# Kernel tuning notes

Measured on AMD Instinct MI355X. Metric: run time of the kernel, lower is better.

Reference implementation:

```python
import jax, jax.numpy as jnp
import numpy as np

VOCAB, EMB, HID = 32000, 512, 512
BATCH, SEQ = 32, 512


def setup_inputs() -> dict:
    key = jax.random.key(0)
    ks = jax.random.split(key, 6)
    return {
        "enc_input": jax.random.randint(ks[0], (BATCH, SEQ), 0, VOCAB),
        "emb": jax.random.normal(ks[1], (VOCAB, EMB), dtype=jnp.float32) * 0.02,
        "W_ih": jax.random.normal(ks[2], (2, 3 * HID, EMB), dtype=jnp.float32) * 0.05,
        "W_hh": jax.random.normal(ks[3], (2, 3 * HID, HID), dtype=jnp.float32) * 0.05,
        "b_ih": jax.random.normal(ks[4], (2, 3 * HID), dtype=jnp.float32) * 0.05,
        "b_hh": jax.random.normal(ks[5], (2, 3 * HID), dtype=jnp.float32) * 0.05,
    }


def _gru_dir(gx, W_hh_d, b_hh_d, H):
    # gx: [B, S, 3H] precomputed input gates; scan left-to-right over S.
    B = gx.shape[0]

    def step(h, gxt):
        gh = h @ W_hh_d.T + b_hh_d  # [B, 3H]
        r = jax.nn.sigmoid(gxt[:, :H] + gh[:, :H])
        z = jax.nn.sigmoid(gxt[:, H:2 * H] + gh[:, H:2 * H])
        n = jnp.tanh(gxt[:, 2 * H:] + r * gh[:, 2 * H:])
        h_new = (1.0 - z) * n + z * h
        return h_new, h_new

    h0 = jnp.zeros((B, H), dtype=gx.dtype)
    hT, ys = jax.lax.scan(step, h0, jnp.swapaxes(gx, 0, 1))  # ys: [S, B, H]
    return jnp.swapaxes(ys, 0, 1), hT


def reference(enc_input, emb, W_ih, W_hh, b_ih, b_hh):
    # NOTE: original torch code feeds the bidirectional GRU one timestep at a
    # time, so BOTH directions effectively run left-to-right over the sequence
    # (each with its own weights). We reproduce that exact behavior.
    H = W_hh.shape[-1]
    x = emb[enc_input]  # [B, S, E]
    # Precompute input-gate projections for both directions in one einsum.
    gx = jnp.einsum('bse,dge->bsdg', x, W_ih) + b_ih  # [B, S, 2, 3H]
    out0, h0 = _gru_dir(gx[:, :, 0, :], W_hh[0], b_hh[0], H)
    out1, h1 = _gru_dir(gx[:, :, 1, :], W_hh[1], b_hh[1], H)
    encoded = jnp.concatenate([out0, out1], axis=-1)  # [B, S, 2H]
    hidden = jnp.stack([h0, h1], axis=0)  # [2, B, H]
    return encoded, hidden
```

## Files before the change

### kernel.cpp

```cpp
#include <hip/hip_runtime.h>
#include <stdint.h>

#define VOCAB 32000
#define EMBD 512
#define HID 512
#define BATCH 32
#define SEQL 512

typedef short bf16x8 __attribute__((ext_vector_type(8)));
typedef short bf16x4 __attribute__((ext_vector_type(4)));
typedef float f32x4 __attribute__((ext_vector_type(4)));

#define AGENT __HIP_MEMORY_SCOPE_AGENT
#define RLX __ATOMIC_RELAXED

static __device__ __forceinline__ float bf2f(short u) {
  union { unsigned u; float f; } c;
  c.u = ((unsigned)(unsigned short)u) << 16;
  return c.f;
}
static __device__ __forceinline__ unsigned short f2bf(float f) {
  union { float f; unsigned u; } c;
  c.f = f;
  unsigned x = c.u;
  unsigned r = (x + 0x7fffu + ((x >> 16) & 1u)) >> 16;
  return (unsigned short)r;
}

__global__ __launch_bounds__(256) void cvt_f32_bf16(
    const float* __restrict__ src, unsigned short* __restrict__ dst, int n8) {
  int i = blockIdx.x * 256 + threadIdx.x;
  if (i >= n8) return;
  const float4* s = (const float4*)src + (size_t)i * 2;
  float4 a = s[0], b = s[1];
  uint4 p;
  p.x = (unsigned)f2bf(a.x) | ((unsigned)f2bf(a.y) << 16);
  p.y = (unsigned)f2bf(a.z) | ((unsigned)f2bf(a.w) << 16);
  p.z = (unsigned)f2bf(b.x) | ((unsigned)f2bf(b.y) << 16);
  p.w = (unsigned)f2bf(b.z) | ((unsigned)f2bf(b.w) << 16);
  ((uint4*)dst)[i] = p;
}

#define GBM 128
#define GBN 128
#define GBK 64

__global__ __launch_bounds__(256) void gemm_gx(
    const int* __restrict__ enc,
    const unsigned short* __restrict__ embb,
    const unsigned short* __restrict__ wih,
    const float* __restrict__ b_ih,
    unsigned short* __restrict__ gx)
{
  __shared__ __align__(16) unsigned short As[GBM * GBK];
  __shared__ __align__(16) unsigned short Bs[GBN * GBK];
  __shared__ int tokl[GBM];

  const int n0 = blockIdx.x * GBN;
  const int m0 = blockIdx.y * GBM;
  const int tid = threadIdx.x;
  if (tid < GBM) {
    int m = m0 + tid;
    tokl[tid] = enc[(m & 31) * SEQL + (m >> 5)];
  }
  __syncthreads();

  const int l = tid & 63, w = tid >> 6;
  const int wr = w >> 1, wc = w & 1;

  f32x4 acc[4][4];
  f32x4 zero = {0.f, 0.f, 0.f, 0.f};
#pragma unroll
  for (int mt = 0; mt < 4; ++mt)
#pragma unroll
    for (int nt = 0; nt < 4; ++nt) acc[mt][nt] = zero;

  for (int kt = 0; kt < 512; kt += GBK) {
#pragma unroll
    for (int it = 0; it < 4; ++it) {
      int c = it * 256 + tid;
      int r = c >> 3, kc = c & 7;
      uint4 v = *(const uint4*)(embb + (size_t)tokl[r] * 512 + kt + kc * 8);
      unsigned off = (unsigned)(r * 128 + kc * 16); off ^= (r & 7) << 4;
      *(uint4*)((char*)As + off) = v;
    }
#pragma unroll
    for (int it = 0; it < 4; ++it) {
      int c = it * 256 + tid;
      int r = c >> 3, kc = c & 7;
      uint4 v = *(const uint4*)(wih + (size_t)(n0 + r) * 512 + kt + kc * 8);
      unsigned off = (unsigned)(r * 128 + kc * 16); off ^= (r & 7) << 4;
      *(uint4*)((char*)Bs + off) = v;
    }
    __syncthreads();
#pragma unroll
    for (int ks = 0; ks < 2; ++ks) {
      bf16x8 af[4], bfr[4];
#pragma unroll
      for (int mt = 0; mt < 4; ++mt) {
        int r = wr * 64 + mt * 16 + (l & 15);
        unsigned off = (unsigned)(r * 128 + ks * 64 + (l >> 4) * 16);
        off ^= (r & 7) << 4;
        af[mt] = *(const bf16x8*)((char*)As + off);
      }
#pragma unroll
      for (int nt = 0; nt < 4; ++nt) {
        int r = wc * 64 + nt * 16 + (l & 15);
        unsigned off = (unsigned)(r * 128 + ks * 64 + (l >> 4) * 16);
        off ^= (r & 7) << 4;
        bfr[nt] = *(const bf16x8*)((char*)Bs + off);
      }
#pragma unroll
      for (int mt = 0; mt < 4; ++mt)
#pragma unroll
        for (int nt = 0; nt < 4; ++nt)
          acc[mt][nt] = __builtin_amdgcn_mfma_f32_16x16x32_bf16(
              af[mt], bfr[nt], acc[mt][nt], 0, 0, 0);
    }
    __syncthreads();
  }

#pragma unroll
  for (int nt = 0; nt < 4; ++nt) {
    int n = n0 + wc * 64 + nt * 16 + (l & 15);
    int d = n >= 1536 ? 1 : 0;
    int g = n - d * 1536;
    float bias = b_ih[n];
#pragma unroll
    for (int mt = 0; mt < 4; ++mt) {
      int mbase = m0 + wr * 64 + mt * 16 + (l >> 4) * 4;
      int s = mbase >> 5;
      int b = mbase & 31;
      unsigned v0 = (unsigned)f2bf(acc[mt][nt][0] + bias) |
                    ((unsigned)f2bf(acc[mt][nt][1] + bias) << 16);
      unsigned v1 = (unsigned)f2bf(acc[mt][nt][2] + bias) |
                    ((unsigned)f2bf(acc[mt][nt][3] + bias) << 16);
      size_t off = ((size_t)(s * 2 + d) * 1536 + g) * 32 + b;
      uint2 pv; pv.x = v0; pv.y = v1;
      *(uint2*)(gx + off) = pv;
    }
  }
}

#define JW 16

__global__ __launch_bounds__(128) void scan_gru(
    const unsigned short* __restrict__ gx,
    const unsigned short* __restrict__ whh,
    const float* __restrict__ bhh,
    unsigned short* __restrict__ hbuf,
    unsigned* __restrict__ flags,
    float* __restrict__ out)
{
  __shared__ __align__(16) unsigned short Wl[48 * 512];

  const int bid = blockIdx.x;
  const int d = bid >> 5;
  const int wg = bid & 31;
  const int j0 = wg * JW;
  const int tid = threadIdx.x;
  const int l = tid & 63;
  const int w = tid >> 6;

  for (int it = 0; it < 24; ++it) {
    int c = it * 128 + tid;
    int lr = c >> 6, kc = c & 63;
    int gate = lr >> 4, jj = lr & 15;
    uint4 v = *(const uint4*)(whh +
        (size_t)(d * 1536 + gate * 512 + j0 + jj) * 512 + kc * 8);
    unsigned off = (unsigned)(lr * 1024 + kc * 16); off ^= (lr & 7) << 4;
    *(uint4*)((char*)Wl + off) = v;
  }

  const int jl = l & 15;
  const int jglob = j0 + jl;
  const int b0 = w * 16;
  const int brow = b0 + (l >> 4) * 4;
  const float bh_r = bhh[d * 1536 + jglob];
  const float bh_z = bhh[d * 1536 + 512 + jglob];
  const float bh_n = bhh[d * 1536 + 1024 + jglob];

  unsigned* myflag = flags + ((size_t)(d * 2 + w) * 32 + wg) * 16;
  const unsigned* fbase = flags + (size_t)(d * 2 + w) * 32 * 16;

  float hold[4] = {0.f, 0.f, 0.f, 0.f};

  __syncthreads();

  bf16x4 gr, gz, gn;
  {
    size_t gb = (size_t)d * 1536 * 32;
    gr = *(const bf16x4*)(gx + gb + (size_t)jglob * 32 + brow);
    gz = *(const bf16x4*)(gx + gb + (size_t)(512 + jglob) * 32 + brow);
    gn = *(const bf16x4*)(gx + gb + (size_t)(1024 + jglob) * 32 + brow);
  }

  for (int t = 0; t < SEQL; ++t) {
    f32x4 accr = {0.f, 0.f, 0.f, 0.f};
    f32x4 accz = accr, accn = accr;

    if (t > 0) {
      const unsigned tagv = (unsigned)t;
      for (;;) {
        unsigned fv = tagv;
        if (l < 32)
          fv = __hip_atomic_load(fbase + (size_t)l * 16, RLX, AGENT);
        if (__ballot(fv >= tagv) == ~0ull) break;
        __builtin_amdgcn_s_sleep(1);
      }
      const unsigned long long* hq = (const unsigned long long*)
          (hbuf + (size_t)(d * 2 + ((t - 1) & 1)) * 32 * 512);
      size_t qb = (size_t)(b0 + (l & 15)) * 128 + (l >> 4) * 2;
      union { unsigned long long q[2]; bf16x8 v; } afu[16];
#pragma unroll
      for (int ks = 0; ks < 16; ++ks) {
        afu[ks].q[0] = __hip_atomic_load(hq + qb + ks * 8, RLX, AGENT);
        afu[ks].q[1] = __hip_atomic_load(hq + qb + ks * 8 + 1, RLX, AGENT);
      }
#pragma unroll
      for (int ks = 0; ks < 16; ++ks) {
        unsigned kb = (unsigned)(ks * 64 + (l >> 4) * 16);
        unsigned r0 = (unsigned)jl, r1 = (unsigned)(16 + jl), r2 = (unsigned)(32 + jl);
        bf16x8 bR = *(const bf16x8*)((char*)Wl + ((r0 * 1024 + kb) ^ ((r0 & 7) << 4)));
        bf16x8 bZ = *(const bf16x8*)((char*)Wl + ((r1 * 1024 + kb) ^ ((r1 & 7) << 4)));
        bf16x8 bN = *(const bf16x8*)((char*)Wl + ((r2 * 1024 + kb) ^ ((r2 & 7) << 4)));
        accr = __builtin_amdgcn_mfma_f32_16x16x32_bf16(afu[ks].v, bR, accr, 0, 0, 0);
        accz = __builtin_amdgcn_mfma_f32_16x16x32_bf16(afu[ks].v, bZ, accz, 0, 0, 0);
        accn = __builtin_amdgcn_mfma_f32_16x16x32_bf16(afu[ks].v, bN, accn, 0, 0, 0);
      }
    }

#pragma unroll
    for (int i = 0; i < 4; ++i) {
      float ghr = accr[i] + bh_r;
      float ghz = accz[i] + bh_z;
      float ghn = accn[i] + bh_n;
      float pr = bf2f(gr[i]) + ghr;
      float pz = bf2f(gz[i]) + ghz;
      float r = 1.f / (1.f + __expf(-pr));
      float z = 1.f / (1.f + __expf(-pz));
      float n = tanhf(bf2f(gn[i]) + r * ghn);
      hold[i] = (1.f - z) * n + z * hold[i];
    }

    if (t < SEQL - 1) {
      unsigned* hn32 = (unsigned*)(hbuf + (size_t)(d * 2 + (t & 1)) * 32 * 512);
      unsigned mybf[4], pare[4];
#pragma unroll
      for (int i = 0; i < 4; ++i) mybf[i] = f2bf(hold[i]);
#pragma unroll
      for (int i = 0; i < 4; ++i) {
        unsigned ot = (unsigned)__shfl_xor((int)mybf[i], 1);
        pare[i] = (jl & 1) ? (ot | (mybf[i] << 16)) : (mybf[i] | (ot << 16));
      }
      int jc2 = (j0 + (jl & ~1)) >> 1;
      int i0 = (jl & 1) ? 2 : 0;
      __hip_atomic_store(hn32 + (size_t)(brow + i0) * 256 + jc2, pare[i0],
                         RLX, AGENT);
      __hip_atomic_store(hn32 + (size_t)(brow + i0 + 1) * 256 + jc2,
                         pare[i0 + 1], RLX, AGENT);
      asm volatile("s_waitcnt vmcnt(0)" ::: "memory");
      if (l == 0)
        __hip_atomic_store(myflag, (unsigned)(t + 1), RLX, AGENT);
    }

#pragma unroll
    for (int i = 0; i < 4; ++i)
      out[((size_t)(brow + i) * SEQL + t) * 1024 + d * 512 + jglob] = hold[i];
    if (t == SEQL - 1) {
#pragma unroll
      for (int i = 0; i < 4; ++i)
        out[(size_t)BATCH * SEQL * 1024 +
            (size_t)(d * 32 + brow + i) * 512 + jglob] = hold[i];
    }

    if (t < SEQL - 1) {
      size_t gb = ((size_t)(t + 1) * 2 + d) * 1536 * 32;
      gr = *(const bf16x4*)(gx + gb + (size_t)jglob * 32 + brow);
      gz = *(const bf16x4*)(gx + gb + (size_t)(512 + jglob) * 32 + brow);
      gn = *(const bf16x4*)(gx + gb + (size_t)(1024 + jglob) * 32 + brow);
    }
  }
}

extern "C" void kernel_launch(void* const* d_in, const int* in_sizes, int n_in,
                              void* d_out, int out_size, void* d_ws, size_t ws_size,
                              hipStream_t stream) {
  const int* enc = (const int*)d_in[0];
  const float* emb = (const float*)d_in[1];
  const float* wih = (const float*)d_in[2];
  const float* whh = (const float*)d_in[3];
  const float* bih = (const float*)d_in[4];
  const float* bhh = (const float*)d_in[5];
  float* out = (float*)d_out;

  char* ws = (char*)d_ws;
  unsigned* flags = (unsigned*)ws;
  unsigned short* hbuf = (unsigned short*)(ws + 8192);
  unsigned short* whh_b = (unsigned short*)(ws + 139264);
  unsigned short* wih_b = (unsigned short*)(ws + 139264 + 3145728);
  unsigned short* emb_b = (unsigned short*)(ws + 139264 + 2 * 3145728);
  unsigned short* gx = (unsigned short*)(ws + 139264 + 2 * 3145728 + 32768000);

  hipMemsetAsync(flags, 0, 8192, stream);
  cvt_f32_bf16<<<768, 256, 0, stream>>>(whh, whh_b, 196608);
  cvt_f32_bf16<<<768, 256, 0, stream>>>(wih, wih_b, 196608);
  cvt_f32_bf16<<<8000, 256, 0, stream>>>(emb, emb_b, 2048000);
  gemm_gx<<<dim3(24, 128), 256, 0, stream>>>(enc, emb_b, wih_b, bih, gx);
  scan_gru<<<64, 128, 0, stream>>>(gx, whh_b, bhh, hbuf, flags, out);
}
```

Measured before the change: 1.991 ms.

## Halve scan workgroups by giving each 32 hidden units per direction

The persistent GRU scan kernel now runs 16 workgroups per direction instead of 32. Each workgroup owns 32 hidden columns, holds twice as much W_hh in LDS (96 KB) and issues twice the MFMAs per step. This halves the number of flags each wave polls in the per-step cross-workgroup barrier, cutting synchronization latency. In exchange, per-step compute on the serial critical path doubles for each workgroup and fewer CUs share the matmul.

```diff
diff --git a/kernel.cpp b/kernel.cpp
--- a/kernel.cpp
+++ b/kernel.cpp
@@ -142,7 +142,8 @@
   }
 }
 
-#define JW 16
+#define JW 32
+#define NWGD 16
 
 __global__ __launch_bounds__(128) void scan_gru(
     const unsigned short* __restrict__ gx,
@@ -152,20 +153,20 @@
     unsigned* __restrict__ flags,
     float* __restrict__ out)
 {
-  __shared__ __align__(16) unsigned short Wl[48 * 512];
+  __shared__ __align__(16) unsigned short Wl[96 * 512];
 
   const int bid = blockIdx.x;
-  const int d = bid >> 5;
-  const int wg = bid & 31;
+  const int d = bid >> 4;
+  const int wg = bid & 15;
   const int j0 = wg * JW;
   const int tid = threadIdx.x;
   const int l = tid & 63;
   const int w = tid >> 6;
 
-  for (int it = 0; it < 24; ++it) {
+  for (int it = 0; it < 48; ++it) {
     int c = it * 128 + tid;
     int lr = c >> 6, kc = c & 63;
-    int gate = lr >> 4, jj = lr & 15;
+    int gate = lr >> 5, jj = lr & 31;
     uint4 v = *(const uint4*)(whh +
         (size_t)(d * 1536 + gate * 512 + j0 + jj) * 512 + kc * 8);
     unsigned off = (unsigned)(lr * 1024 + kc * 16); off ^= (lr & 7) << 4;
@@ -173,37 +174,49 @@
   }
 
   const int jl = l & 15;
-  const int jglob = j0 + jl;
   const int b0 = w * 16;
   const int brow = b0 + (l >> 4) * 4;
-  const float bh_r = bhh[d * 1536 + jglob];
-  const float bh_z = bhh[d * 1536 + 512 + jglob];
-  const float bh_n = bhh[d * 1536 + 1024 + jglob];
-
-  unsigned* myflag = flags + ((size_t)(d * 2 + w) * 32 + wg) * 16;
-  const unsigned* fbase = flags + (size_t)(d * 2 + w) * 32 * 16;
-
-  float hold[4] = {0.f, 0.f, 0.f, 0.f};
+  float bh_r[2], bh_z[2], bh_n[2];
+#pragma unroll
+  for (int jt = 0; jt < 2; ++jt) {
+    int jg = j0 + jt * 16 + jl;
+    bh_r[jt] = bhh[d * 1536 + jg];
+    bh_z[jt] = bhh[d * 1536 + 512 + jg];
+    bh_n[jt] = bhh[d * 1536 + 1024 + jg];
+  }
+
+  unsigned* myflag = flags + ((size_t)(d * 2 + w) * NWGD + wg) * 16;
+  const unsigned* fbase = flags + (size_t)(d * 2 + w) * NWGD * 16;
+
+  float hold[2][4] = {{0.f, 0.f, 0.f, 0.f}, {0.f, 0.f, 0.f, 0.f}};
 
   __syncthreads();
 
-  bf16x4 gr, gz, gn;
+  bf16x4 gr[2], gz[2], gn[2];
   {
     size_t gb = (size_t)d * 1536 * 32;
-    gr = *(const bf16x4*)(gx + gb + (size_t)jglob * 32 + brow);
-    gz = *(const bf16x4*)(gx + gb + (size_t)(512 + jglob) * 32 + brow);
-    gn = *(const bf16x4*)(gx + gb + (size_t)(1024 + jglob) * 32 + brow);
+#pragma unroll
+    for (int jt = 0; jt < 2; ++jt) {
+      int jg = j0 + jt * 16 + jl;
+      gr[jt] = *(const bf16x4*)(gx + gb + (size_t)jg * 32 + brow);
+      gz[jt] = *(const bf16x4*)(gx + gb + (size_t)(512 + jg) * 32 + brow);
+      gn[jt] = *(const bf16x4*)(gx + gb + (size_t)(1024 + jg) * 32 + brow);
+    }
   }
 
   for (int t = 0; t < SEQL; ++t) {
-    f32x4 accr = {0.f, 0.f, 0.f, 0.f};
-    f32x4 accz = accr, accn = accr;
+    f32x4 zero = {0.f, 0.f, 0.f, 0.f};
+    f32x4 acc[2][3];
+#pragma unroll
+    for (int jt = 0; jt < 2; ++jt)
+#pragma unroll
+      for (int g = 0; g < 3; ++g) acc[jt][g] = zero;
 
     if (t > 0) {
       const unsigned tagv = (unsigned)t;
       for (;;) {
         unsigned fv = tagv;
-        if (l < 32)
+        if (l < NWGD)
           fv = __hip_atomic_load(fbase + (size_t)l * 16, RLX, AGENT);
         if (__ballot(fv >= tagv) == ~0ull) break;
         __builtin_amdgcn_s_sleep(1);
@@ -220,65 +233,86 @@
 #pragma unroll
       for (int ks = 0; ks < 16; ++ks) {
         unsigned kb = (unsigned)(ks * 64 + (l >> 4) * 16);
-        unsigned r0 = (unsigned)jl, r1 = (unsigned)(16 + jl), r2 = (unsigned)(32 + jl);
-        bf16x8 bR = *(const bf16x8*)((char*)Wl + ((r0 * 1024 + kb) ^ ((r0 & 7) << 4)));
-        bf16x8 bZ = *(const bf16x8*)((char*)Wl + ((r1 * 1024 + kb) ^ ((r1 & 7) << 4)));
-        bf16x8 bN = *(const bf16x8*)((char*)Wl + ((r2 * 1024 + kb) ^ ((r2 & 7) << 4)));
-        accr = __builtin_amdgcn_mfma_f32_16x16x32_bf16(afu[ks].v, bR, accr, 0, 0, 0);
-        accz = __builtin_amdgcn_mfma_f32_16x16x32_bf16(afu[ks].v, bZ, accz, 0, 0, 0);
-        accn = __builtin_amdgcn_mfma_f32_16x16x32_bf16(afu[ks].v, bN, accn, 0, 0, 0);
-      }
-    }
-
-#pragma unroll
-    for (int i = 0; i < 4; ++i) {
-      float ghr = accr[i] + bh_r;
-      float ghz = accz[i] + bh_z;
-      float ghn = accn[i] + bh_n;
-      float pr = bf2f(gr[i]) + ghr;
-      float pz = bf2f(gz[i]) + ghz;
-      float r = 1.f / (1.f + __expf(-pr));
-      float z = 1.f / (1.f + __expf(-pz));
-      float n = tanhf(bf2f(gn[i]) + r * ghn);
-      hold[i] = (1.f - z) * n + z * hold[i];
-    }
+#pragma unroll
+        for (int jt = 0; jt < 2; ++jt)
+#pragma unroll
+          for (int g = 0; g < 3; ++g) {
+            unsigned r = (unsigned)(g * 32 + jt * 16 + jl);
+            bf16x8 bW = *(const bf16x8*)((char*)Wl +
+                ((r * 1024 + kb) ^ ((r & 7) << 4)));
+            acc[jt][g] = __builtin_amdgcn_mfma_f32_16x16x32_bf16(
+                afu[ks].v, bW, acc[jt][g], 0, 0, 0);
+          }
+      }
+    }
+
+#pragma unroll
+    for (int jt = 0; jt < 2; ++jt)
+#pragma unroll
+      for (int i = 0; i < 4; ++i) {
+        float ghr = acc[jt][0][i] + bh_r[jt];
+        float ghz = acc[jt][1][i] + bh_z[jt];
+        float ghn = acc[jt][2][i] + bh_n[jt];
+        float pr = bf2f(gr[jt][i]) + ghr;
+        float pz = bf2f(gz[jt][i]) + ghz;
+        float r = 1.f / (1.f + __expf(-pr));
+        float z = 1.f / (1.f + __expf(-pz));
+        float n = tanhf(bf2f(gn[jt][i]) + r * ghn);
+        hold[jt][i] = (1.f - z) * n + z * hold[jt][i];
+      }
 
     if (t < SEQL - 1) {
       unsigned* hn32 = (unsigned*)(hbuf + (size_t)(d * 2 + (t & 1)) * 32 * 512);
-      unsigned mybf[4], pare[4];
-#pragma unroll
-      for (int i = 0; i < 4; ++i) mybf[i] = f2bf(hold[i]);
-#pragma unroll
-      for (int i = 0; i < 4; ++i) {
-        unsigned ot = (unsigned)__shfl_xor((int)mybf[i], 1);
-        pare[i] = (jl & 1) ? (ot | (mybf[i] << 16)) : (mybf[i] | (ot << 16));
-      }
-      int jc2 = (j0 + (jl & ~1)) >> 1;
-      int i0 = (jl & 1) ? 2 : 0;
-      __hip_atomic_store(hn32 + (size_t)(brow + i0) * 256 + jc2, pare[i0],
-                         RLX, AGENT);
-      __hip_atomic_store(hn32 + (size_t)(brow + i0 + 1) * 256 + jc2,
-                         pare[i0 + 1], RLX, AGENT);
+#pragma unroll
+      for (int jt = 0; jt < 2; ++jt) {
+        unsigned mybf[4], pare[4];
+#pragma unroll
+        for (int i = 0; i < 4; ++i) mybf[i] = f2bf(hold[jt][i]);
+#pragma unroll
+        for (int i = 0; i < 4; ++i) {
+          unsigned ot = (unsigned)__shfl_xor((int)mybf[i], 1);
+          pare[i] = (jl & 1) ? (ot | (mybf[i] << 16)) : (mybf[i] | (ot << 16));
+        }
+        int jc2 = (j0 + jt * 16 + (jl & ~1)) >> 1;
+        int i0 = (jl & 1) ? 2 : 0;
+        __hip_atomic_store(hn32 + (size_t)(brow + i0) * 256 + jc2, pare[i0],
+                           RLX, AGENT);
+        __hip_atomic_store(hn32 + (size_t)(brow + i0 + 1) * 256 + jc2,
+                           pare[i0 + 1], RLX, AGENT);
+      }
       asm volatile("s_waitcnt vmcnt(0)" ::: "memory");
       if (l == 0)
         __hip_atomic_store(myflag, (unsigned)(t + 1), RLX, AGENT);
     }
 
 #pragma unroll
-    for (int i = 0; i < 4; ++i)
-      out[((size_t)(brow + i) * SEQL + t) * 1024 + d * 512 + jglob] = hold[i];
+    for (int jt = 0; jt < 2; ++jt) {
+      int jg = j0 + jt * 16 + jl;
+#pragma unroll
+      for (int i = 0; i < 4; ++i)
+        out[((size_t)(brow + i) * SEQL + t) * 1024 + d * 512 + jg] =
+            hold[jt][i];
+    }
     if (t == SEQL - 1) {
 #pragma unroll
-      for (int i = 0; i < 4; ++i)
-        out[(size_t)BATCH * SEQL * 1024 +
-            (size_t)(d * 32 + brow + i) * 512 + jglob] = hold[i];
+      for (int jt = 0; jt < 2; ++jt) {
+        int jg = j0 + jt * 16 + jl;
+#pragma unroll
+        for (int i = 0; i < 4; ++i)
+          out[(size_t)BATCH * SEQL * 1024 +
+              (size_t)(d * 32 + brow + i) * 512 + jg] = hold[jt][i];
+      }
     }
 
     if (t < SEQL - 1) {
       size_t gb = ((size_t)(t + 1) * 2 + d) * 1536 * 32;
-      gr = *(const bf16x4*)(gx + gb + (size_t)jglob * 32 + brow);
-      gz = *(const bf16x4*)(gx + gb + (size_t)(512 + jglob) * 32 + brow);
-      gn = *(const bf16x4*)(gx + gb + (size_t)(1024 + jglob) * 32 + brow);
+#pragma unroll
+      for (int jt = 0; jt < 2; ++jt) {
+        int jg = j0 + jt * 16 + jl;
+        gr[jt] = *(const bf16x4*)(gx + gb + (size_t)jg * 32 + brow);
+        gz[jt] = *(const bf16x4*)(gx + gb + (size_t)(512 + jg) * 32 + brow);
+        gn[jt] = *(const bf16x4*)(gx + gb + (size_t)(1024 + jg) * 32 + brow);
+      }
     }
   }
 }
@@ -307,5 +341,5 @@
   cvt_f32_bf16<<<768, 256, 0, stream>>>(wih, wih_b, 196608);
   cvt_f32_bf16<<<8000, 256, 0, stream>>>(emb, emb_b, 2048000);
   gemm_gx<<<dim3(24, 128), 256, 0, stream>>>(enc, emb_b, wih_b, bih, gx);
-  scan_gru<<<64, 128, 0, stream>>>(gx, whh_b, bhh, hbuf, flags, out);
-}
+  scan_gru<<<32, 128, 0, stream>>>(gx, whh_b, bhh, hbuf, flags, out);
+}
```

Result: slower. 2.419 ms (+21.5%).
